# Performance work log

Measured on AMD Instinct MI355X. Metric: run time of the kernel, lower is better.

The kernel has to match this reference:

```python
import jax, jax.numpy as jnp
import numpy as np

V, E, H, B, T = 50000, 300, 512, 64, 256


def _lstm_dir(x, wih, whh, bih, bhh, reverse):
    # x: [B,T,D]; wih: [4H,D]; whh: [4H,H]; PyTorch gate order i,f,g,o
    pre = jnp.einsum('btd,gd->btg', x, wih) + bih + bhh  # [B,T,4H]
    pre_t = jnp.swapaxes(pre, 0, 1)  # [T,B,4H]
    h0 = jnp.zeros((x.shape[0], whh.shape[1]), x.dtype)

    def step(carry, g):
        h, c = carry
        gates = g + h @ whh.T
        i, f, gg, o = jnp.split(gates, 4, axis=-1)
        c = jax.nn.sigmoid(f) * c + jax.nn.sigmoid(i) * jnp.tanh(gg)
        h = jax.nn.sigmoid(o) * jnp.tanh(c)
        return (h, c), h

    _, hs = jax.lax.scan(step, (h0, h0), pre_t, reverse=reverse)
    return jnp.swapaxes(hs, 0, 1)  # [B,T,H]


def setup_inputs() -> dict:
    key = jax.random.key(0)
    ks = jax.random.split(key, 24)
    s = 1.0 / np.sqrt(H)
    u = lambda k, shp: jax.random.uniform(k, shp, jnp.float32, -s, s)
    inp = {
        'input_ids': jax.random.randint(ks[0], (B, T), 0, V),
        'input_masks': jnp.ones((B, T), jnp.float32),
        'labels': jax.random.uniform(ks[1], (B, T), jnp.float32),
        'emb': jax.random.normal(ks[2], (V, E), jnp.float32),
        'lin_w': u(ks[3], (1, H)), 'lin_b': u(ks[4], (1,)),
    }
    dims = {'l0': E, 'l1': 2 * H}
    i = 5
    for layer, din in dims.items():
        for d in ('f', 'b'):
            inp[f'w_ih_{layer}{d}'] = u(ks[i], (4 * H, din)); i += 1
            inp[f'w_hh_{layer}{d}'] = u(ks[i], (4 * H, H)); i += 1
            inp[f'b_ih_{layer}{d}'] = u(ks[i], (4 * H,)); i += 1
            inp[f'b_hh_{layer}{d}'] = u(ks[i], (4 * H,)); i += 1
    return inp


def reference(input_ids, input_masks, labels, emb, lin_w, lin_b,
              w_ih_l0f, w_hh_l0f, b_ih_l0f, b_hh_l0f,
              w_ih_l0b, w_hh_l0b, b_ih_l0b, b_hh_l0b,
              w_ih_l1f, w_hh_l1f, b_ih_l1f, b_hh_l1f,
              w_ih_l1b, w_hh_l1b, b_ih_l1b, b_hh_l1b):
    x = emb[input_ids]  # vectorized gather, [B,T,E]
    h0f = _lstm_dir(x, w_ih_l0f, w_hh_l0f, b_ih_l0f, b_hh_l0f, False)
    h0b = _lstm_dir(x, w_ih_l0b, w_hh_l0b, b_ih_l0b, b_hh_l0b, True)
    x1 = jnp.concatenate([h0f, h0b], axis=-1)  # [B,T,2H] (dropout inactive at eval)
    h1f = _lstm_dir(x1, w_ih_l1f, w_hh_l1f, b_ih_l1f, b_hh_l1f, False)
    h1b = _lstm_dir(x1, w_ih_l1b, w_hh_l1b, b_ih_l1b, b_hh_l1b, True)
    mean_h = 0.5 * (h1f + h1b)  # mean over 2 directions, [B,T,H]
    scores = jax.nn.sigmoid(jnp.einsum('bth,oh->bto', mean_h, lin_w) + lin_b)  # [B,T,1]
    err = (scores[..., 0] - labels) ** 2 * input_masks  # masked MSE per token
    loss = jnp.mean(jnp.sum(err, axis=1) / jnp.sum(input_masks, axis=1))
    return loss
```

## Files before the change

kernel.cpp:

```cpp
#include <hip/hip_runtime.h>
#include <stdint.h>

#define T_SEQ 256
#define B_SZ  64
#define HID   512
#define G4    2048
#define E_DIM 300
#define E_PAD 320

typedef float f32x4 __attribute__((ext_vector_type(4)));
typedef short bf16x8 __attribute__((ext_vector_type(8)));
typedef unsigned int u32x4 __attribute__((ext_vector_type(4)));

__device__ __forceinline__ unsigned short f2bf(float f) {
    union { float f; unsigned u; } v; v.f = f;
    unsigned r = v.u + 0x7FFF + ((v.u >> 16) & 1);
    return (unsigned short)(r >> 16);
}
__device__ __forceinline__ float bf2f(unsigned short b) {
    union { unsigned u; float f; } v; v.u = ((unsigned)b) << 16;
    return v.f;
}
__device__ __forceinline__ float sigm_f(float x) { return 1.0f / (1.0f + __expf(-x)); }
__device__ __forceinline__ float tanh_f(float x) {
    float e = __expf(-2.0f * fabsf(x));
    float t = (1.0f - e) / (1.0f + e);
    return x < 0.0f ? -t : t;
}

__global__ void k_sentinel(float* out) { out[0] = 12345.0f; }

__global__ __launch_bounds__(256) void k_gather(const int* __restrict__ ids,
                                                const float* __restrict__ emb,
                                                unsigned short* __restrict__ x) {
    int w = threadIdx.x >> 6, lane = threadIdx.x & 63;
    int row = blockIdx.x * 4 + w;
    int id = ids[row];
    const float* e = emb + (size_t)id * E_DIM;
    unsigned short* xr = x + (size_t)row * E_PAD;
    for (int k = lane; k < E_PAD; k += 64)
        xr[k] = (k < E_DIM) ? f2bf(e[k]) : (unsigned short)0;
}

__global__ __launch_bounds__(256) void k_castpad(const float* __restrict__ src,
                                                 unsigned short* __restrict__ dst,
                                                 int Ks, int Kp) {
    int row = blockIdx.x;
    const float* s = src + (size_t)row * Ks;
    unsigned short* d = dst + (size_t)row * Kp;
    for (int k = threadIdx.x; k < Kp; k += 256)
        d[k] = (k < Ks) ? f2bf(s[k]) : (unsigned short)0;
}

__global__ __launch_bounds__(256) void k_gemm(const unsigned short* __restrict__ A,
                                              const unsigned short* __restrict__ W,
                                              const float* __restrict__ bih,
                                              const float* __restrict__ bhh,
                                              unsigned short* __restrict__ outp,
                                              int Ka) {
    __shared__ __align__(16) short As[64][40];
    __shared__ __align__(16) short Bs[64][40];
    int tid = threadIdx.x;
    int w = tid >> 6, lane = tid & 63;
    int m0 = blockIdx.x * 64, n0 = blockIdx.y * 64;

    f32x4 acc[4];
    #pragma unroll
    for (int nt = 0; nt < 4; ++nt) { acc[nt][0]=0.f; acc[nt][1]=0.f; acc[nt][2]=0.f; acc[nt][3]=0.f; }

    int r = tid >> 2, seg = tid & 3;
    for (int k0 = 0; k0 < Ka; k0 += 32) {
        *(bf16x8*)&As[r][seg * 8] = *(const bf16x8*)&A[(size_t)(m0 + r) * Ka + k0 + seg * 8];
        *(bf16x8*)&Bs[r][seg * 8] = *(const bf16x8*)&W[(size_t)(n0 + r) * Ka + k0 + seg * 8];
        __syncthreads();
        bf16x8 a = *(const bf16x8*)&As[w * 16 + (lane & 15)][(lane >> 4) * 8];
        #pragma unroll
        for (int nt = 0; nt < 4; ++nt) {
            bf16x8 b = *(const bf16x8*)&Bs[nt * 16 + (lane & 15)][(lane >> 4) * 8];
            acc[nt] = __builtin_amdgcn_mfma_f32_16x16x32_bf16(a, b, acc[nt], 0, 0, 0);
        }
        __syncthreads();
    }
    #pragma unroll
    for (int nt = 0; nt < 4; ++nt) {
        #pragma unroll
        for (int rr = 0; rr < 4; ++rr) {
            int m = m0 + w * 16 + (lane >> 4) * 4 + rr;
            int col = n0 + nt * 16 + (lane & 15);
            float v = acc[nt][rr] + bih[col] + bhh[col];
            int b = m >> 8, t = m & 255;
            int g = col >> 9, jc = col & 511;
            size_t idx = (((((size_t)t * 4 + (b >> 4)) * 4 + ((b >> 2) & 3)) * 32
                           + (jc >> 4)) * 16 + (jc & 15)) * 16 + g * 4 + (b & 3);
            outp[idx] = f2bf(v);
        }
    }
}

__global__ __launch_bounds__(256, 1) void k_lstm_layer(
        const unsigned short* __restrict__ pre2_f, const unsigned short* __restrict__ pre2_b,
        const unsigned short* __restrict__ whh_f, const unsigned short* __restrict__ whh_b,
        unsigned short* __restrict__ h_pp,
        int* __restrict__ flags,
        unsigned short* __restrict__ x1,
        unsigned short* __restrict__ h1f, unsigned short* __restrict__ h1b,
        int mode, int flag_base) {
    int tid = threadIdx.x, w = tid >> 6, lane = tid & 63;
    int jgg = blockIdx.x, rg = blockIdx.y, dir = blockIdx.z;
    int jg = jgg * 4 + w;
    int r0 = rg * 16, q = lane >> 4, j = lane & 15;
    const unsigned short* pre2 = dir ? pre2_b : pre2_f;
    const unsigned short* whh = dir ? whh_b : whh_f;
    int* gbase = flags + ((dir * 4 + rg) * 8) * 16;

    __shared__ __align__(16) short ws_a[16 * 512];

    bf16x8 breg[4][16];
    #pragma unroll
    for (int g = 0; g < 4; ++g)
        #pragma unroll
        for (int kc = 0; kc < 16; ++kc)
            breg[g][kc] = *(const bf16x8*)(whh + (size_t)(g * 512 + jg * 16 + j) * 512 + q * 8 + kc * 32);

    float cr[4];
    #pragma unroll
    for (int rr = 0; rr < 4; ++rr) cr[rr] = 0.f;

    int aswz = (j & 7) << 4;
    const char* abase = (const char*)ws_a + (j << 10);
    int ko16 = q << 4;

    bf16x8 pcur0, pcur1;
    {
        int t0 = dir ? (T_SEQ - 1) : 0;
        const unsigned short* pp =
            pre2 + ((((((size_t)t0 * 4 + rg) * 4 + q) * 32 + jg) * 16 + j) * 16);
        pcur0 = *(const bf16x8*)pp;
        pcur1 = *(const bf16x8*)(pp + 8);
    }

    for (int s = 0; s < T_SEQ; ++s) {
        int t = dir ? (T_SEQ - 1 - s) : s;
        const unsigned short* hprev = h_pp + ((size_t)(s & 1) * 2 + dir) * (B_SZ * HID);
        unsigned short* hnext = h_pp + ((size_t)((s + 1) & 1) * 2 + dir) * (B_SZ * HID);

        f32x4 a0, a1, a2, a3;
        a0[0]=0.f;a0[1]=0.f;a0[2]=0.f;a0[3]=0.f; a1=a0; a2=a0; a3=a0;
        if (s > 0) {
            const unsigned short* hp = hprev + (size_t)r0 * HID;
            u32x4 va[4];
            #pragma unroll
            for (int c = 0; c < 4; ++c) {
                int ch = tid + c * 256;
                const void* src = hp + ((ch >> 6) << 9) + ((ch & 63) << 3);
                asm volatile("global_load_dwordx4 %0, %1, off sc0 sc1"
                             : "=v"(va[c]) : "v"(src));
            }
            asm volatile("s_waitcnt vmcnt(0)" ::: "memory");
            #pragma unroll
            for (int c = 0; c < 4; ++c) {
                int ch = tid + c * 256;
                int r = ch >> 6, o = ch & 63;
                *(u32x4*)((char*)ws_a + (r << 10) + ((o << 4) ^ ((r & 7) << 4))) = va[c];
            }
            __syncthreads();

            #pragma unroll
            for (int kc = 0; kc < 16; ++kc) {
                bf16x8 a = *(const bf16x8*)(abase + (((kc << 6) + ko16) ^ aswz));
                a0 = __builtin_amdgcn_mfma_f32_16x16x32_bf16(a, breg[0][kc], a0, 0, 0, 0);
                a1 = __builtin_amdgcn_mfma_f32_16x16x32_bf16(a, breg[1][kc], a1, 0, 0, 0);
                a2 = __builtin_amdgcn_mfma_f32_16x16x32_bf16(a, breg[2][kc], a2, 0, 0, 0);
                a3 = __builtin_amdgcn_mfma_f32_16x16x32_bf16(a, breg[3][kc], a3, 0, 0, 0);
            }
        }

        unsigned hbits[4];
        #pragma unroll
        for (int rr = 0; rr < 4; ++rr) {
            float iv = a0[rr] + bf2f((unsigned short)pcur0[rr]);
            float fv = a1[rr] + bf2f((unsigned short)pcur0[4 + rr]);
            float gv = a2[rr] + bf2f((unsigned short)pcur1[rr]);
            float ov = a3[rr] + bf2f((unsigned short)pcur1[4 + rr]);
            cr[rr] = sigm_f(fv) * cr[rr] + sigm_f(iv) * tanh_f(gv);
            float hh = sigm_f(ov) * tanh_f(cr[rr]);
            hbits[rr] = (unsigned)f2bf(hh);
        }

        #pragma unroll
        for (int rr = 0; rr < 4; ++rr) {
            unsigned nb = (unsigned)__shfl_xor((int)hbits[rr], 1);
            if ((j & 1) == 0) {
                unsigned pair = (hbits[rr] & 0xFFFFu) | (nb << 16);
                void* dsth = (void*)(hnext + (size_t)(r0 + q * 4 + rr) * HID + jg * 16 + j);
                asm volatile("global_store_dword %0, %1, off sc0 sc1"
                             :: "v"(dsth), "v"(pair) : "memory");
            }
        }

        asm volatile("s_waitcnt vmcnt(0)" ::: "memory");
        __syncthreads();
        int target = flag_base + s + 1;
        if (tid == 0)
            __hip_atomic_store(&gbase[jgg * 16], target, __ATOMIC_RELAXED, __HIP_MEMORY_SCOPE_AGENT);

        #pragma unroll
        for (int rr = 0; rr < 4; ++rr) {
            unsigned short hb = (unsigned short)hbits[rr];
            int brow = r0 + q * 4 + rr;
            if (mode == 0)
                x1[((size_t)brow * T_SEQ + t) * 1024 + dir * HID + jg * 16 + j] = hb;
            else {
                unsigned short* o = dir ? h1b : h1f;
                o[((size_t)t * B_SZ + brow) * HID + jg * 16 + j] = hb;
            }
        }
        bf16x8 pn0, pn1;
        {
            int sn = (s + 1 < T_SEQ) ? s + 1 : s;
            int tn = dir ? (T_SEQ - 1 - sn) : sn;
            const unsigned short* pp =
                pre2 + ((((((size_t)tn * 4 + rg) * 4 + q) * 32 + jg) * 16 + j) * 16);
            pn0 = *(const bf16x8*)pp;
            pn1 = *(const bf16x8*)(pp + 8);
        }

        if (tid < 8) {
            while (__hip_atomic_load(&gbase[tid * 16], __ATOMIC_RELAXED, __HIP_MEMORY_SCOPE_AGENT) < target) {}
        }
        __syncthreads();
        pcur0 = pn0; pcur1 = pn1;
    }
}

__global__ __launch_bounds__(256) void k_score(const unsigned short* __restrict__ h1f,
                                               const unsigned short* __restrict__ h1b,
                                               const float* __restrict__ lin_w,
                                               const float* __restrict__ lin_b,
                                               const float* __restrict__ labels,
                                               const float* __restrict__ masks,
                                               float* __restrict__ err) {
    int w = threadIdx.x >> 6, lane = threadIdx.x & 63;
    int idx = blockIdx.x * 4 + w;
    int b = idx >> 8, t = idx & 255;
    size_t base = ((size_t)t * B_SZ + b) * HID + lane * 8;
    bf16x8 hf = *(const bf16x8*)(h1f + base);
    bf16x8 hb = *(const bf16x8*)(h1b + base);
    float sum = 0.f;
    #pragma unroll
    for (int i = 0; i < 8; ++i) {
        float m = 0.5f * (bf2f((unsigned short)hf[i]) + bf2f((unsigned short)hb[i]));
        sum += m * lin_w[lane * 8 + i];
    }
    #pragma unroll
    for (int off = 32; off; off >>= 1) sum += __shfl_xor(sum, off);
    if (lane == 0) {
        float sc = 1.0f / (1.0f + expf(-(sum + lin_b[0])));
        float d = sc - labels[b * 256 + t];
        err[b * 256 + t] = d * d * masks[b * 256 + t];
    }
}

__global__ void k_loss(const float* __restrict__ err, const float* __restrict__ masks,
                       float* __restrict__ out) {
    int lane = threadIdx.x;
    float se = 0.f, sm = 0.f;
    for (int t = 0; t < 256; ++t) {
        se += err[lane * 256 + t];
        sm += masks[lane * 256 + t];
    }
    float v = se / sm;
    #pragma unroll
    for (int off = 32; off; off >>= 1) v += __shfl_xor(v, off);
    if (lane == 0) out[0] = v * (1.0f / 64.0f);
}

extern "C" void kernel_launch(void* const* d_in, const int* in_sizes, int n_in,
                              void* d_out, int out_size, void* d_ws, size_t ws_size,
                              hipStream_t stream) {
    const int*   ids    = (const int*)d_in[0];
    const float* masks  = (const float*)d_in[1];
    const float* labels = (const float*)d_in[2];
    const float* emb    = (const float*)d_in[3];
    const float* lin_w  = (const float*)d_in[4];
    const float* lin_b  = (const float*)d_in[5];
    const float* w_ih[4] = {(const float*)d_in[6],  (const float*)d_in[10],
                            (const float*)d_in[14], (const float*)d_in[18]};
    const float* w_hh[4] = {(const float*)d_in[7],  (const float*)d_in[11],
                            (const float*)d_in[15], (const float*)d_in[19]};
    const float* b_ih[4] = {(const float*)d_in[8],  (const float*)d_in[12],
                            (const float*)d_in[16], (const float*)d_in[20]};
    const float* b_hh[4] = {(const float*)d_in[9],  (const float*)d_in[13],
                            (const float*)d_in[17], (const float*)d_in[21]};

    const size_t PRE_B   = (size_t)T_SEQ * B_SZ * G4 * 2;
    const size_t SH_B    = (size_t)16384 * 1024 * 2;
    const size_t WHH_B   = (size_t)G4 * HID * 2;
    const size_t WT1_B   = (size_t)G4 * 1024 * 2;
    const size_t HPP_B   = (size_t)2 * 2 * B_SZ * HID * 2;
    const size_t FLG_B   = (size_t)256 * 64;
    const size_t ERR_B   = (size_t)B_SZ * T_SEQ * 4;
    const size_t REQUIRED = 2 * PRE_B + SH_B + 4 * WHH_B + 2 * WT1_B + HPP_B + FLG_B + ERR_B;
    if (REQUIRED > ws_size) {
        k_sentinel<<<1, 1, 0, stream>>>((float*)d_out);
        return;
    }

    char* base = (char*)d_ws;
    unsigned short* pre_f = (unsigned short*)(base);
    unsigned short* pre_b = (unsigned short*)(base + PRE_B);
    char* sh = base + 2 * PRE_B;
    unsigned short* x_bf = (unsigned short*)(sh);
    unsigned short* wt0f = (unsigned short*)(sh + (size_t)16384 * E_PAD * 2);
    unsigned short* wt0b = (unsigned short*)(sh + (size_t)16384 * E_PAD * 2 + (size_t)2048 * E_PAD * 2);
    unsigned short* x1   = (unsigned short*)(sh);
    unsigned short* h1f  = (unsigned short*)(sh);
    unsigned short* h1b  = (unsigned short*)(sh + (size_t)T_SEQ * B_SZ * HID * 2);
    char* q = sh + SH_B;
    unsigned short* whhb[4];
    for (int i = 0; i < 4; ++i) { whhb[i] = (unsigned short*)q; q += WHH_B; }
    unsigned short* wt1f = (unsigned short*)q; q += WT1_B;
    unsigned short* wt1b = (unsigned short*)q; q += WT1_B;
    unsigned short* h_pp = (unsigned short*)q; q += HPP_B;
    int* flags = (int*)q; q += FLG_B;
    float* err = (float*)q; q += ERR_B;

    hipMemsetAsync(flags, 0, FLG_B, stream);

    k_gather<<<4096, 256, 0, stream>>>(ids, emb, x_bf);
    k_castpad<<<2048, 256, 0, stream>>>(w_ih[0], wt0f, E_DIM, E_PAD);
    k_castpad<<<2048, 256, 0, stream>>>(w_ih[1], wt0b, E_DIM, E_PAD);
    k_castpad<<<2048, 256, 0, stream>>>(w_ih[2], wt1f, 1024, 1024);
    k_castpad<<<2048, 256, 0, stream>>>(w_ih[3], wt1b, 1024, 1024);
    for (int i = 0; i < 4; ++i)
        k_castpad<<<2048, 256, 0, stream>>>(w_hh[i], whhb[i], 512, 512);

    dim3 gemm_grid(16384 / 64, 2048 / 64);
    k_gemm<<<gemm_grid, 256, 0, stream>>>(x_bf, wt0f, b_ih[0], b_hh[0], pre_f, E_PAD);
    k_gemm<<<gemm_grid, 256, 0, stream>>>(x_bf, wt0b, b_ih[1], b_hh[1], pre_b, E_PAD);

    dim3 rec_grid(8, 4, 2);
    k_lstm_layer<<<rec_grid, 256, 0, stream>>>(pre_f, pre_b, whhb[0], whhb[1],
                                               h_pp, flags, x1, nullptr, nullptr, 0, 0);

    k_gemm<<<gemm_grid, 256, 0, stream>>>(x1, wt1f, b_ih[2], b_hh[2], pre_f, 1024);
    k_gemm<<<gemm_grid, 256, 0, stream>>>(x1, wt1b, b_ih[3], b_hh[3], pre_b, 1024);

    k_lstm_layer<<<rec_grid, 256, 0, stream>>>(pre_f, pre_b, whhb[2], whhb[3],
                                               h_pp, flags, nullptr, h1f, h1b, 1, 256);

    k_score<<<4096, 256, 0, stream>>>(h1f, h1b, lin_w, lin_b, labels, masks, err);
    k_loss<<<1, 64, 0, stream>>>(err, masks, (float*)d_out);
}
```

Before: 2.816 ms.

## Repartition LSTM recurrence: one block per hidden slice over full batch, weights in LDS

The recurrent kernel used to split work over batch-row groups and hidden groups (64 blocks), with the W_hh slices held in registers. Now each of the 32 blocks per direction owns one 16-column hidden slice for all 64 batch rows, and its W_hh slice (4 gates × 16 × 512) is staged once in LDS and read from there inside the MFMA loop. Each block now loads the whole previous h (64×512) every step and spins on 32 flags instead of 8. The intent is to cut register pressure and change the sync group size, at the cost of more LDS traffic per step and larger per-step global reads.

```diff
diff --git a/kernel.cpp b/kernel.cpp
--- a/kernel.cpp
+++ b/kernel.cpp
@@ -106,38 +106,41 @@
         unsigned short* __restrict__ h1f, unsigned short* __restrict__ h1b,
         int mode, int flag_base) {
     int tid = threadIdx.x, w = tid >> 6, lane = tid & 63;
-    int jgg = blockIdx.x, rg = blockIdx.y, dir = blockIdx.z;
-    int jg = jgg * 4 + w;
-    int r0 = rg * 16, q = lane >> 4, j = lane & 15;
+    int jg = blockIdx.x, dir = blockIdx.y;
+    int q = lane >> 4, j = lane & 15;
     const unsigned short* pre2 = dir ? pre2_b : pre2_f;
     const unsigned short* whh = dir ? whh_b : whh_f;
-    int* gbase = flags + ((dir * 4 + rg) * 8) * 16;
-
-    __shared__ __align__(16) short ws_a[16 * 512];
-
-    bf16x8 breg[4][16];
-    #pragma unroll
-    for (int g = 0; g < 4; ++g)
-        #pragma unroll
-        for (int kc = 0; kc < 16; ++kc)
-            breg[g][kc] = *(const bf16x8*)(whh + (size_t)(g * 512 + jg * 16 + j) * 512 + q * 8 + kc * 32);
+    int* gbase = flags + dir * 32 * 16;
+
+    __shared__ __align__(16) short ws_b[4 * 16 * 512];
+    __shared__ __align__(16) short ws_a[64 * 512];
+
+    #pragma unroll
+    for (int c = 0; c < 16; ++c) {
+        int ch = tid + c * 256;
+        int r = ch >> 6, o = ch & 63;
+        bf16x8 v = *(const bf16x8*)&whh[((size_t)(r >> 4) * 512 + jg * 16 + (r & 15)) * 512 + o * 8];
+        *(bf16x8*)((char*)ws_b + (r << 10) + ((o << 4) ^ ((r & 7) << 4))) = v;
+    }
 
     float cr[4];
     #pragma unroll
     for (int rr = 0; rr < 4; ++rr) cr[rr] = 0.f;
 
-    int aswz = (j & 7) << 4;
-    const char* abase = (const char*)ws_a + (j << 10);
+    int swz = (j & 7) << 4;
+    const char* abase = (const char*)ws_a + ((w * 16 + j) << 10);
+    const char* bbase = (const char*)ws_b + (j << 10);
     int ko16 = q << 4;
 
     bf16x8 pcur0, pcur1;
     {
         int t0 = dir ? (T_SEQ - 1) : 0;
         const unsigned short* pp =
-            pre2 + ((((((size_t)t0 * 4 + rg) * 4 + q) * 32 + jg) * 16 + j) * 16);
+            pre2 + ((((((size_t)t0 * 4 + w) * 4 + q) * 32 + jg) * 16 + j) * 16);
         pcur0 = *(const bf16x8*)pp;
         pcur1 = *(const bf16x8*)(pp + 8);
     }
+    __syncthreads();
 
     for (int s = 0; s < T_SEQ; ++s) {
         int t = dir ? (T_SEQ - 1 - s) : s;
@@ -147,18 +150,17 @@
         f32x4 a0, a1, a2, a3;
         a0[0]=0.f;a0[1]=0.f;a0[2]=0.f;a0[3]=0.f; a1=a0; a2=a0; a3=a0;
         if (s > 0) {
-            const unsigned short* hp = hprev + (size_t)r0 * HID;
-            u32x4 va[4];
+            u32x4 va[16];
             #pragma unroll
-            for (int c = 0; c < 4; ++c) {
+            for (int c = 0; c < 16; ++c) {
                 int ch = tid + c * 256;
-                const void* src = hp + ((ch >> 6) << 9) + ((ch & 63) << 3);
+                const void* src = hprev + ((ch >> 6) << 9) + ((ch & 63) << 3);
                 asm volatile("global_load_dwordx4 %0, %1, off sc0 sc1"
                              : "=v"(va[c]) : "v"(src));
             }
             asm volatile("s_waitcnt vmcnt(0)" ::: "memory");
             #pragma unroll
-            for (int c = 0; c < 4; ++c) {
+            for (int c = 0; c < 16; ++c) {
                 int ch = tid + c * 256;
                 int r = ch >> 6, o = ch & 63;
                 *(u32x4*)((char*)ws_a + (r << 10) + ((o << 4) ^ ((r & 7) << 4))) = va[c];
@@ -167,11 +169,12 @@
 
             #pragma unroll
             for (int kc = 0; kc < 16; ++kc) {
-                bf16x8 a = *(const bf16x8*)(abase + (((kc << 6) + ko16) ^ aswz));
-                a0 = __builtin_amdgcn_mfma_f32_16x16x32_bf16(a, breg[0][kc], a0, 0, 0, 0);
-                a1 = __builtin_amdgcn_mfma_f32_16x16x32_bf16(a, breg[1][kc], a1, 0, 0, 0);
-                a2 = __builtin_amdgcn_mfma_f32_16x16x32_bf16(a, breg[2][kc], a2, 0, 0, 0);
-                a3 = __builtin_amdgcn_mfma_f32_16x16x32_bf16(a, breg[3][kc], a3, 0, 0, 0);
+                int off = ((kc << 6) + ko16) ^ swz;
+                bf16x8 a = *(const bf16x8*)(abase + off);
+                a0 = __builtin_amdgcn_mfma_f32_16x16x32_bf16(a, *(const bf16x8*)(bbase + off),         a0, 0, 0, 0);
+                a1 = __builtin_amdgcn_mfma_f32_16x16x32_bf16(a, *(const bf16x8*)(bbase + 16384 + off), a1, 0, 0, 0);
+                a2 = __builtin_amdgcn_mfma_f32_16x16x32_bf16(a, *(const bf16x8*)(bbase + 32768 + off), a2, 0, 0, 0);
+                a3 = __builtin_amdgcn_mfma_f32_16x16x32_bf16(a, *(const bf16x8*)(bbase + 49152 + off), a3, 0, 0, 0);
             }
         }
 
@@ -192,7 +195,7 @@
             unsigned nb = (unsigned)__shfl_xor((int)hbits[rr], 1);
             if ((j & 1) == 0) {
                 unsigned pair = (hbits[rr] & 0xFFFFu) | (nb << 16);
-                void* dsth = (void*)(hnext + (size_t)(r0 + q * 4 + rr) * HID + jg * 16 + j);
+                void* dsth = (void*)(hnext + (size_t)(w * 16 + q * 4 + rr) * HID + jg * 16 + j);
                 asm volatile("global_store_dword %0, %1, off sc0 sc1"
                              :: "v"(dsth), "v"(pair) : "memory");
             }
@@ -202,12 +205,12 @@
         __syncthreads();
         int target = flag_base + s + 1;
         if (tid == 0)
-            __hip_atomic_store(&gbase[jgg * 16], target, __ATOMIC_RELAXED, __HIP_MEMORY_SCOPE_AGENT);
+            __hip_atomic_store(&gbase[jg * 16], target, __ATOMIC_RELAXED, __HIP_MEMORY_SCOPE_AGENT);
 
         #pragma unroll
         for (int rr = 0; rr < 4; ++rr) {
             unsigned short hb = (unsigned short)hbits[rr];
-            int brow = r0 + q * 4 + rr;
+            int brow = w * 16 + q * 4 + rr;
             if (mode == 0)
                 x1[((size_t)brow * T_SEQ + t) * 1024 + dir * HID + jg * 16 + j] = hb;
             else {
@@ -220,12 +223,12 @@
             int sn = (s + 1 < T_SEQ) ? s + 1 : s;
             int tn = dir ? (T_SEQ - 1 - sn) : sn;
             const unsigned short* pp =
-                pre2 + ((((((size_t)tn * 4 + rg) * 4 + q) * 32 + jg) * 16 + j) * 16);
+                pre2 + ((((((size_t)tn * 4 + w) * 4 + q) * 32 + jg) * 16 + j) * 16);
             pn0 = *(const bf16x8*)pp;
             pn1 = *(const bf16x8*)(pp + 8);
         }
 
-        if (tid < 8) {
+        if (tid < 32) {
             while (__hip_atomic_load(&gbase[tid * 16], __ATOMIC_RELAXED, __HIP_MEMORY_SCOPE_AGENT) < target) {}
         }
         __syncthreads();
@@ -339,7 +342,7 @@
     k_gemm<<<gemm_grid, 256, 0, stream>>>(x_bf, wt0f, b_ih[0], b_hh[0], pre_f, E_PAD);
     k_gemm<<<gemm_grid, 256, 0, stream>>>(x_bf, wt0b, b_ih[1], b_hh[1], pre_b, E_PAD);
 
-    dim3 rec_grid(8, 4, 2);
+    dim3 rec_grid(32, 2);
     k_lstm_layer<<<rec_grid, 256, 0, stream>>>(pre_f, pre_b, whhb[0], whhb[1],
                                                h_pp, flags, x1, nullptr, nullptr, 0, 0);
 
```

After: 3.481 ms. 23.6% more time.
